# Performance work log

Measured on AMD Instinct MI355X. Metric: run time of the kernel, lower is better.

Reference implementation:

```python
import jax, jax.numpy as jnp
import numpy as np

EMBED_DIM = 1024
NUM_HEADS = 16
HEAD_DIM = EMBED_DIM // NUM_HEADS  # 64
SCALING = 0.125
T, B = 2048, 2


def setup_inputs() -> dict:
    key = jax.random.key(0)
    k_q, k_len, k_w1, k_b1, k_w2, k_b2 = jax.random.split(key, 6)
    query = jax.random.normal(k_q, (T, B, EMBED_DIM), dtype=jnp.float32)
    # realistic padding: each sequence has a valid length in [T//2, T)
    lengths = jax.random.randint(k_len, (B,), T // 2, T)
    key_padding_mask = jnp.arange(T)[None, :] >= lengths[:, None]  # [B, T] bool, True = pad
    s1 = 1.0 / np.sqrt(EMBED_DIM)
    W_in = jax.random.uniform(k_w1, (3 * EMBED_DIM, EMBED_DIM), jnp.float32, -s1, s1)
    b_in = jax.random.uniform(k_b1, (3 * EMBED_DIM,), jnp.float32, -s1, s1)
    W_out = jax.random.uniform(k_w2, (EMBED_DIM, EMBED_DIM), jnp.float32, -s1, s1)
    b_out = jax.random.uniform(k_b2, (EMBED_DIM,), jnp.float32, -s1, s1)
    return {"query": query, "key_padding_mask": key_padding_mask,
            "W_in": W_in, "b_in": b_in, "W_out": W_out, "b_out": b_out}


def reference(query, key_padding_mask, W_in, b_in, W_out, b_out):
    # query: [T, B, E]; key_padding_mask: [B, S] bool (True = padded key)
    t, b, e = query.shape
    h, hd = NUM_HEADS, HEAD_DIM
    proj = query @ W_in.T + b_in                      # [T, B, 3E]
    q, k, v = jnp.split(proj, 3, axis=-1)             # each [T, B, E]
    q = q * SCALING

    def to_bh(x):  # [T, B, E] -> [B*H, T, hd], matching torch view+transpose
        return x.reshape(t, b * h, hd).transpose(1, 0, 2)

    q, k, v = to_bh(q), to_bh(k), to_bh(v)
    attn_weights = jnp.einsum('bth,bsh->bts', q, k)   # [B*H, T, S]
    attn_weights = attn_weights.reshape(b, h, t, t)
    attn_weights = jnp.where(key_padding_mask[:, None, None, :], -jnp.inf, attn_weights)
    # softmax computed in float32 then cast back, as in the original
    attn_weights = jax.nn.softmax(attn_weights.astype(jnp.float32), axis=-1).astype(query.dtype)
    # dropout p=0 (eval/inference) -> identity
    attn = jnp.einsum('bhts,bhsd->bhtd', attn_weights, v.reshape(b, h, t, hd))  # [B,H,T,hd]
    attn = attn.reshape(b * h, t, hd).transpose(1, 0, 2).reshape(t, b, e)       # [T,B,E]
    return attn @ W_out.T + b_out
```

## Files before the change

kernel.cpp:

```cpp
#include <hip/hip_runtime.h>
#include <hip/hip_bf16.h>
#include <stdint.h>
#include <stddef.h>

typedef __hip_bfloat16 bf16;
typedef __attribute__((ext_vector_type(4))) float f32x4;
typedef __attribute__((ext_vector_type(8))) short s16x8;
typedef __attribute__((ext_vector_type(4))) short s16x4;

#define AS1 __attribute__((address_space(1)))
#define AS3 __attribute__((address_space(3)))

__device__ __forceinline__ void async_ld16(const void* g, void* l) {
  __builtin_amdgcn_global_load_lds((AS1 void*)g, (AS3 void*)l, 16, 0, 0);
}

#if __has_builtin(__builtin_amdgcn_exp2f)
#define EXP2F(x) __builtin_amdgcn_exp2f(x)
#else
#define EXP2F(x) exp2f(x)
#endif

__device__ __forceinline__ unsigned pk_bf16(float a, float b) {
  unsigned ua = __builtin_bit_cast(unsigned, a);
  unsigned ub = __builtin_bit_cast(unsigned, b);
  ua += 0x7FFFu + ((ua >> 16) & 1u);
  ub += 0x7FFFu + ((ub >> 16) & 1u);
  return (ua >> 16) | (ub & 0xFFFF0000u);
}

__device__ __forceinline__ unsigned pk_trunc(float a, float b) {
  return __builtin_amdgcn_perm(__builtin_bit_cast(unsigned, b),
                               __builtin_bit_cast(unsigned, a), 0x07060302u);
}

__global__ __launch_bounds__(256) void convert_all_kernel(const float* __restrict__ q_src,
                                                          const float* __restrict__ wi_src,
                                                          const float* __restrict__ wo_src,
                                                          bf16* __restrict__ q_dst,
                                                          bf16* __restrict__ wi_dst,
                                                          bf16* __restrict__ wo_dst,
                                                          const void* __restrict__ mask,
                                                          int* __restrict__ lengths) {
  int blk = blockIdx.x;
  if (blk >= 4096) {
    __shared__ int s_any;
    __shared__ int s_cnt[256];
    const int tid = threadIdx.x;
    const int b = blk - 4096;
    const unsigned char* m8 = (const unsigned char*)mask;
    if (tid == 0) s_any = 0;
    __syncthreads();
    int local = 0;
    for (int i = tid; i < 4096; i += 256) local |= m8[i];
    if (local) atomicOr(&s_any, 1);
    __syncthreads();
    int cnt = 0;
    if (s_any) {
      for (int t = tid; t < 2048; t += 256) cnt += (m8[b * 2048 + t] == 0) ? 1 : 0;
    } else {
      const int* m32 = (const int*)mask;
      for (int t = tid; t < 2048; t += 256) cnt += (m32[b * 2048 + t] == 0) ? 1 : 0;
    }
    s_cnt[tid] = cnt;
    __syncthreads();
    for (int s = 128; s > 0; s >>= 1) {
      if (tid < s) s_cnt[tid] += s_cnt[tid + s];
      __syncthreads();
    }
    if (tid == 0) lengths[b] = s_cnt[0];
    return;
  }
  const float* src;
  bf16* dst;
  int base;
  if (blk < 2048)      { src = q_src;  dst = q_dst;  base = blk * 2048; }
  else if (blk < 3584) { src = wi_src; dst = wi_dst; base = (blk - 2048) * 2048; }
  else                 { src = wo_src; dst = wo_dst; base = (blk - 3584) * 2048; }
  int i = base + threadIdx.x * 8;
  float4 a = *(const float4*)(src + i);
  float4 b = *(const float4*)(src + i + 4);
  unsigned u[4];
  u[0] = pk_bf16(a.x, a.y); u[1] = pk_bf16(a.z, a.w);
  u[2] = pk_bf16(b.x, b.y); u[3] = pk_bf16(b.z, b.w);
  *(uint4*)(dst + i) = *(const uint4*)u;
}

__global__ __launch_bounds__(256, 5) void gemm_qkv(const bf16* __restrict__ X,
                                                   const bf16* __restrict__ W,
                                                   const float* __restrict__ bias,
                                                   bf16* __restrict__ Qd,
                                                   bf16* __restrict__ Kd,
                                                   bf16* __restrict__ Vt) {
  __shared__ bf16 smem[(64 + 128) * 64];
  bf16* As = smem;
  bf16* Bs = smem + 4096;
  const int K = 1024;
  const int id = blockIdx.x;
  const int mt = id & 63, nt = id >> 6;
  const int m0 = mt * 64, n0 = nt * 128;
  const int tid = threadIdx.x;
  const int wave = tid >> 6, lane = tid & 63;
  const int col = lane & 15, quad = lane >> 4;
  const int wm = wave & 1, wn = wave >> 1;

  f32x4 acc[2][4];
#pragma unroll
  for (int mi = 0; mi < 2; mi++)
#pragma unroll
    for (int ni = 0; ni < 4; ni++) acc[mi][ni] = (f32x4){0.f, 0.f, 0.f, 0.f};

  const bf16* gA[2];
  char* ldA[2];
#pragma unroll
  for (int i = 0; i < 2; i++) {
    const int c = tid + 256 * i;
    const int row = c >> 3;
    const int j = (c & 7) ^ (row & 7);
    gA[i] = X + (size_t)(m0 + row) * K + j * 8;
    ldA[i] = (char*)As + (size_t)(wave * 64 + 256 * i) * 16;
  }
  const bf16* gB[4];
  char* ldB[4];
#pragma unroll
  for (int i = 0; i < 4; i++) {
    const int c = tid + 256 * i;
    const int row = c >> 3;
    const int j = (c & 7) ^ (row & 7);
    gB[i] = W + (size_t)(n0 + row) * K + j * 8;
    ldB[i] = (char*)Bs + (size_t)(wave * 64 + 256 * i) * 16;
  }

  for (int k0 = 0; k0 < K; k0 += 64) {
#pragma unroll
    for (int i = 0; i < 2; i++) async_ld16(gA[i] + k0, ldA[i]);
#pragma unroll
    for (int i = 0; i < 4; i++) async_ld16(gB[i] + k0, ldB[i]);
    __syncthreads();
#pragma unroll
    for (int kh = 0; kh < 2; kh++) {
      s16x8 af[2], bfr[4];
#pragma unroll
      for (int mi = 0; mi < 2; mi++) {
        const int arow = wm * 32 + mi * 16 + col;
        af[mi] = *(const s16x8*)((char*)As + arow * 128 + ((((kh << 2) | quad) ^ (arow & 7)) << 4));
      }
#pragma unroll
      for (int ni = 0; ni < 4; ni++) {
        const int brow = wn * 64 + ni * 16 + col;
        bfr[ni] = *(const s16x8*)((char*)Bs + brow * 128 + ((((kh << 2) | quad) ^ (brow & 7)) << 4));
      }
#pragma unroll
      for (int mi = 0; mi < 2; mi++)
#pragma unroll
        for (int ni = 0; ni < 4; ni++)
          acc[mi][ni] = __builtin_amdgcn_mfma_f32_16x16x32_bf16(af[mi], bfr[ni], acc[mi][ni], 0, 0, 0);
    }
    __syncthreads();
  }

  const float QSCALE = 0.125f * 1.4426950408889634f;
  if (nt < 16) {
    bf16* dstb = (nt < 8) ? Qd : Kd;
    const float sc = (nt < 8) ? QSCALE : 1.0f;
#pragma unroll
    for (int mi = 0; mi < 2; mi++)
#pragma unroll
      for (int ni = 0; ni < 4; ni++)
#pragma unroll
        for (int r = 0; r < 4; r++) {
          int m = m0 + wm * 32 + mi * 16 + quad * 4 + r;
          int n = n0 + wn * 64 + ni * 16 + col;
          float v = (acc[mi][ni][r] + bias[n]) * sc;
          int e = n & 1023, hh = e >> 6, d = e & 63;
          int t = m >> 1, b = m & 1;
          int bh = b * 16 + hh;
          dstb[((size_t)bh * 2048 + t) * 64 + d] = __float2bfloat16(v);
        }
  } else {
    const int hh0 = (nt - 16) * 2;
#pragma unroll
    for (int mi = 0; mi < 2; mi++) {
      const int s0 = wm * 16 + mi * 8 + quad * 2;
      const int off0 = ((s0 >> 2) & 3) * 8 + (s0 >> 4) * 4 + (s0 & 3);
#pragma unroll
      for (int ni = 0; ni < 4; ni++) {
        const int n = n0 + wn * 64 + ni * 16 + col;
        const float bv = bias[n];
        const int dfull = wn * 64 + ni * 16 + col;
        const int hh_rel = dfull >> 6, dd = dfull & 63;
#pragma unroll
        for (int b = 0; b < 2; b++) {
          float v0 = acc[mi][ni][b] + bv;
          float v1 = acc[mi][ni][b + 2] + bv;
          const int p = b * 2 + hh_rel;
          *(unsigned*)((char*)smem + ((p * 2048) + dd * 32 + off0) * 2) = pk_bf16(v0, v1);
        }
      }
    }
    __syncthreads();
    const int bh = (wave >> 1) * 16 + hh0 + (wave & 1);
    bf16* dstp = Vt + (size_t)bh * 131072 + mt * 2048;
    const char* srcp = (const char*)smem + wave * 4096;
#pragma unroll
    for (int jj = 0; jj < 4; jj++) {
      s16x8 v = *(const s16x8*)(srcp + jj * 1024 + lane * 16);
      *(s16x8*)(dstp + jj * 512 + lane * 8) = v;
    }
  }
}

__global__ __launch_bounds__(512, 4) void attn_kernel(const bf16* __restrict__ Qd,
                                                      const bf16* __restrict__ Kd,
                                                      const bf16* __restrict__ Vt,
                                                      const int* __restrict__ lengths,
                                                      bf16* __restrict__ attn_out) {
  __shared__ bf16 Ks[2][2][64 * 64];
  __shared__ bf16 Vs[2][2][64 * 64];

  const int id = blockIdx.x;
  const int slot = id >> 3;
  const int bh = (id & 7) * 4 + (slot & 3);
  const int qt0 = (slot >> 2) * 128;
  const int b = bh >> 4, h = bh & 15;

  const int tid = threadIdx.x;
  const int wave = tid >> 6, lane = tid & 63;
  const int half = wave >> 2, hw = wave & 3;
  const int col = lane & 15, quad = lane >> 4;
  const int len = lengths[b];
  const int nfull = len >> 6;
  const int rem = len & 63;
  const int nkt = nfull + (rem ? 1 : 0);
  const int nh0 = (nkt + 1) >> 1;
  const int first = half ? nh0 : 0;
  const int cnt = half ? (nkt - nh0) : nh0;

  s16x8 bq[2][2];
#pragma unroll
  for (int g = 0; g < 2; g++) {
    const bf16* qptr =
        Qd + ((size_t)bh * 2048 + qt0 + hw * 32 + g * 16 + col) * 64 + quad * 8;
    bq[g][0] = *(const s16x8*)(qptr);
    bq[g][1] = *(const s16x8*)(qptr + 32);
  }

  const int kbase0 = col * 128 + ((quad ^ (col & 7)) << 4);
  const int kbase1 = kbase0 ^ 64;
  const int HBUF = half * 16384;

  const bf16* Kg = Kd + (size_t)bh * 2048 * 64;
  const bf16* Vg = Vt + (size_t)bh * 131072;
  const int c0 = hw * 128 + lane, c1 = c0 + 64;
  const int r0 = c0 >> 3, j0 = (c0 & 7) ^ (r0 & 7);
  const int r1 = c1 >> 3, j1 = (c1 & 7) ^ (r1 & 7);
  const bf16* gK0 = Kg + r0 * 64 + j0 * 8;
  const bf16* gK1 = Kg + r1 * 64 + j1 * 8;
  const bf16* gV0 = Vg + (j0 >> 2) * 2048 + r0 * 32 + (j0 & 3) * 8;
  const bf16* gV1 = Vg + (j1 >> 2) * 2048 + r1 * 32 + (j1 & 3) * 8;
  const int dst0 = (hw * 128) * 16, dst1 = (hw * 128 + 64) * 16;

  auto stage = [&](int kt, int BUF) {
    const int off = kt * 4096;
    async_ld16(gK0 + off, (char*)Ks + BUF + dst0);
    async_ld16(gK1 + off, (char*)Ks + BUF + dst1);
    async_ld16(gV0 + off, (char*)Vs + BUF + dst0);
    async_ld16(gV1 + off, (char*)Vs + BUF + dst1);
  };

  const s16x4 aOnes = {0x3F80, 0x3F80, 0x3F80, 0x3F80};
  const f32x4 Zf = (f32x4){0.f, 0.f, 0.f, 0.f};
  f32x4 lacc[2] = {Zf, Zf};
  f32x4 oaccT[2][4];
#pragma unroll
  for (int g = 0; g < 2; g++)
#pragma unroll
    for (int dt = 0; dt < 4; dt++) oaccT[g][dt] = Zf;

  auto score = [&](int BUF, f32x4 (&s0)[4], f32x4 (&s1)[4]) {
#pragma unroll
    for (int ti = 0; ti < 4; ti++) {
      const s16x8 ak0 = *(const s16x8*)((char*)Ks + BUF + ti * 2048 + kbase0);
      s0[ti] = __builtin_amdgcn_mfma_f32_16x16x32_bf16(ak0, bq[0][0], Zf, 0, 0, 0);
      s1[ti] = __builtin_amdgcn_mfma_f32_16x16x32_bf16(ak0, bq[1][0], Zf, 0, 0, 0);
      const s16x8 ak1 = *(const s16x8*)((char*)Ks + BUF + ti * 2048 + kbase1);
      s0[ti] = __builtin_amdgcn_mfma_f32_16x16x32_bf16(ak1, bq[0][1], s0[ti], 0, 0, 0);
      s1[ti] = __builtin_amdgcn_mfma_f32_16x16x32_bf16(ak1, bq[1][1], s1[ti], 0, 0, 0);
    }
  };
  auto accum = [&](int BUF, s16x4 (&bP0)[4], s16x4 (&bP1)[4]) {
#pragma unroll
    for (int ti = 0; ti < 4; ti++) {
      lacc[0] = __builtin_amdgcn_mfma_f32_16x16x16bf16_1k(aOnes, bP0[ti], lacc[0], 0, 0, 0);
      lacc[1] = __builtin_amdgcn_mfma_f32_16x16x16bf16_1k(aOnes, bP1[ti], lacc[1], 0, 0, 0);
    }
#pragma unroll
    for (int dt = 0; dt < 4; dt++) {
#pragma unroll
      for (int sh = 0; sh < 2; sh++) {
        const s16x8 av = *(const s16x8*)((char*)Vs + BUF + dt * 2048 + (sh ? kbase1 : kbase0));
        const s16x4 alo = __builtin_shufflevector(av, av, 0, 1, 2, 3);
        const s16x4 ahi = __builtin_shufflevector(av, av, 4, 5, 6, 7);
        oaccT[0][dt] = __builtin_amdgcn_mfma_f32_16x16x16bf16_1k(alo, bP0[sh * 2], oaccT[0][dt], 0, 0, 0);
        oaccT[0][dt] = __builtin_amdgcn_mfma_f32_16x16x16bf16_1k(ahi, bP0[sh * 2 + 1], oaccT[0][dt], 0, 0, 0);
        oaccT[1][dt] = __builtin_amdgcn_mfma_f32_16x16x16bf16_1k(alo, bP1[sh * 2], oaccT[1][dt], 0, 0, 0);
        oaccT[1][dt] = __builtin_amdgcn_mfma_f32_16x16x16bf16_1k(ahi, bP1[sh * 2 + 1], oaccT[1][dt], 0, 0, 0);
      }
    }
  };

  auto tile_full = [&](int BUF) {
    f32x4 s0[4], s1[4];
    score(BUF, s0, s1);
    s16x4 bP0[4], bP1[4];
#pragma unroll
    for (int ti = 0; ti < 4; ti++) {
      uint2 u0 = {pk_trunc(EXP2F(s0[ti][0]), EXP2F(s0[ti][1])),
                  pk_trunc(EXP2F(s0[ti][2]), EXP2F(s0[ti][3]))};
      bP0[ti] = __builtin_bit_cast(s16x4, u0);
      uint2 u1 = {pk_trunc(EXP2F(s1[ti][0]), EXP2F(s1[ti][1])),
                  pk_trunc(EXP2F(s1[ti][2]), EXP2F(s1[ti][3]))};
      bP1[ti] = __builtin_bit_cast(s16x4, u1);
    }
    accum(BUF, bP0, bP1);
  };

  auto tile_mask = [&](int BUF) {
    f32x4 s0[4], s1[4];
    score(BUF, s0, s1);
    s16x4 bP0[4], bP1[4];
#pragma unroll
    for (int ti = 0; ti < 4; ti++) {
      const int sb = ti * 16 + quad * 4;
      float a0 = (sb + 0 < rem) ? EXP2F(s0[ti][0]) : 0.f;
      float a1 = (sb + 1 < rem) ? EXP2F(s0[ti][1]) : 0.f;
      float a2 = (sb + 2 < rem) ? EXP2F(s0[ti][2]) : 0.f;
      float a3 = (sb + 3 < rem) ? EXP2F(s0[ti][3]) : 0.f;
      uint2 u0 = {pk_trunc(a0, a1), pk_trunc(a2, a3)};
      bP0[ti] = __builtin_bit_cast(s16x4, u0);
      float c0m = (sb + 0 < rem) ? EXP2F(s1[ti][0]) : 0.f;
      float c1m = (sb + 1 < rem) ? EXP2F(s1[ti][1]) : 0.f;
      float c2m = (sb + 2 < rem) ? EXP2F(s1[ti][2]) : 0.f;
      float c3m = (sb + 3 < rem) ? EXP2F(s1[ti][3]) : 0.f;
      uint2 u1 = {pk_trunc(c0m, c1m), pk_trunc(c2m, c3m)};
      bP1[ti] = __builtin_bit_cast(s16x4, u1);
    }
    accum(BUF, bP0, bP1);
  };

  stage(first, HBUF);
  __syncthreads();
  for (int i = 0; i < nh0; i++) {
    if (i + 1 < cnt) stage(first + i + 1, HBUF + ((i + 1) & 1) * 8192);
    if (i < cnt) {
      const int kt = first + i;
      const int BUF = HBUF + (i & 1) * 8192;
      if (kt < nfull) tile_full(BUF); else tile_mask(BUF);
    }
    __syncthreads();
  }

  float* OF = (float*)Ks;
  float* LF = (float*)Vs;
  const int me = hw * 64 + lane;
  if (half == 1) {
#pragma unroll
    for (int g = 0; g < 2; g++) {
      LF[g * 256 + me] = lacc[g][0];
#pragma unroll
      for (int dt = 0; dt < 4; dt++)
#pragma unroll
        for (int r = 0; r < 4; r++)
          OF[(g * 16 + dt * 4 + r) * 256 + me] = oaccT[g][dt][r];
    }
  }
  __syncthreads();
  if (half == 0) {
#pragma unroll
    for (int g = 0; g < 2; g++) {
      const float linv = 1.0f / (lacc[g][0] + LF[g * 256 + me]);
      const int t = qt0 + hw * 32 + g * 16 + col;
      bf16* outp = attn_out + ((size_t)t * 2 + b) * 1024 + h * 64 + quad * 4;
#pragma unroll
      for (int dt = 0; dt < 4; dt++) {
        float o0 = (oaccT[g][dt][0] + OF[(g * 16 + dt * 4 + 0) * 256 + me]) * linv;
        float o1 = (oaccT[g][dt][1] + OF[(g * 16 + dt * 4 + 1) * 256 + me]) * linv;
        float o2 = (oaccT[g][dt][2] + OF[(g * 16 + dt * 4 + 2) * 256 + me]) * linv;
        float o3 = (oaccT[g][dt][3] + OF[(g * 16 + dt * 4 + 3) * 256 + me]) * linv;
        uint2 u = {pk_bf16(o0, o1), pk_bf16(o2, o3)};
        *(uint2*)(outp + dt * 16) = u;
      }
    }
  }
}

__global__ __launch_bounds__(256) void gemm_out(const bf16* __restrict__ Aa,
                                                const bf16* __restrict__ W,
                                                const float* __restrict__ bias,
                                                float* __restrict__ out) {
  __shared__ bf16 Bs[128 * 64];
  __shared__ bf16 As[64 * 64];
  const int K = 1024;
  const int m0 = blockIdx.y * 64, n0 = blockIdx.x * 128;
  const int tid = threadIdx.x;
  const int wave = tid >> 6, lane = tid & 63;
  const int col = lane & 15, quad = lane >> 4;

  f32x4 acc[8];
#pragma unroll
  for (int ni = 0; ni < 8; ni++) acc[ni] = (f32x4){0.f, 0.f, 0.f, 0.f};

  const bf16* gB[4];
  char* ldsB[4];
#pragma unroll
  for (int i = 0; i < 4; i++) {
    const int c = tid + 256 * i;
    const int row = c >> 3;
    const int j = (c & 7) ^ (row & 7);
    gB[i] = W + (size_t)(n0 + row) * K + j * 8;
    ldsB[i] = (char*)Bs + (size_t)(wave * 64 + 256 * i) * 16;
  }
  const bf16* gA[2];
  char* ldsA[2];
#pragma unroll
  for (int i = 0; i < 2; i++) {
    const int c = tid + 256 * i;
    const int row = c >> 3;
    const int j = (c & 7) ^ (row & 7);
    gA[i] = Aa + (size_t)(m0 + row) * K + j * 8;
    ldsA[i] = (char*)As + (size_t)(wave * 64 + 256 * i) * 16;
  }

  for (int k0 = 0; k0 < K; k0 += 64) {
#pragma unroll
    for (int i = 0; i < 4; i++) async_ld16(gB[i] + k0, ldsB[i]);
#pragma unroll
    for (int i = 0; i < 2; i++) async_ld16(gA[i] + k0, ldsA[i]);
    __syncthreads();
    const int arow = wave * 16 + col;
    const int abase = arow * 128 + ((quad ^ (arow & 7)) << 4);
    const s16x8 af0 = *(const s16x8*)((char*)As + abase);
    const s16x8 af1 = *(const s16x8*)((char*)As + (abase ^ 64));
#pragma unroll
    for (int ni = 0; ni < 8; ni++) {
      const int brow = ni * 16 + col;
      const int bbase = brow * 128 + ((quad ^ (brow & 7)) << 4);
      const s16x8 b0 = *(const s16x8*)((char*)Bs + bbase);
      acc[ni] = __builtin_amdgcn_mfma_f32_16x16x32_bf16(af0, b0, acc[ni], 0, 0, 0);
      const s16x8 b1 = *(const s16x8*)((char*)Bs + (bbase ^ 64));
      acc[ni] = __builtin_amdgcn_mfma_f32_16x16x32_bf16(af1, b1, acc[ni], 0, 0, 0);
    }
    __syncthreads();
  }

#pragma unroll
  for (int ni = 0; ni < 8; ni++)
#pragma unroll
    for (int r = 0; r < 4; r++) {
      int m = m0 + wave * 16 + quad * 4 + r;
      int n = n0 + ni * 16 + col;
      out[(size_t)m * 1024 + n] = acc[ni][r] + bias[n];
    }
}

extern "C" void kernel_launch(void* const* d_in, const int* in_sizes, int n_in,
                              void* d_out, int out_size, void* d_ws, size_t ws_size,
                              hipStream_t stream) {
  (void)in_sizes; (void)n_in; (void)out_size; (void)ws_size;
  const float* query = (const float*)d_in[0];
  const void*  mask  = d_in[1];
  const float* W_in  = (const float*)d_in[2];
  const float* b_in  = (const float*)d_in[3];
  const float* W_out = (const float*)d_in[4];
  const float* b_out = (const float*)d_in[5];
  float* out = (float*)d_out;

  char* ws = (char*)d_ws;
  bf16* Xbf    = (bf16*)(ws);
  bf16* attnb  = (bf16*)(ws);
  bf16* Winbf  = (bf16*)(ws + 8388608);
  bf16* Woutbf = (bf16*)(ws + 8388608 + 6291456);
  bf16* Qd     = (bf16*)(ws + 16777216);
  bf16* Kd     = (bf16*)(ws + 25165824);
  bf16* Vt     = (bf16*)(ws + 33554432);
  int*  lens   = (int*)(ws + 41943040);

  convert_all_kernel<<<4098, 256, 0, stream>>>(query, W_in, W_out, Xbf, Winbf, Woutbf,
                                               mask, lens);
  gemm_qkv<<<1536, 256, 0, stream>>>(Xbf, Winbf, b_in, Qd, Kd, Vt);
  attn_kernel<<<512, 512, 0, stream>>>(Qd, Kd, Vt, lens, attnb);
  gemm_out<<<dim3(8, 64), 256, 0, stream>>>(attnb, Woutbf, b_out, out);
}
```

Before: 183.5 us.

## Shrink output GEMM tile to 64x64 with 2x2 wave layout

Reworks the output-projection GEMM from 64x128 tiles, where each wave owned a 16x128 strip, to 64x64 tiles where each wave owns a 32x32 sub-tile as a 2x2 grid of MFMA blocks. The grid doubles to 1024 blocks to fill more CUs on a 4096x1024 output. LDS per block is halved and launch bounds request 4 blocks per CU for occupancy. The trade-off is more total global/LDS traffic per output element and lower arithmetic intensity per block.

```diff
diff --git a/kernel.cpp b/kernel.cpp
--- a/kernel.cpp
+++ b/kernel.cpp
@@ -394,73 +394,78 @@
   }
 }
 
-__global__ __launch_bounds__(256) void gemm_out(const bf16* __restrict__ Aa,
-                                                const bf16* __restrict__ W,
-                                                const float* __restrict__ bias,
-                                                float* __restrict__ out) {
-  __shared__ bf16 Bs[128 * 64];
+__global__ __launch_bounds__(256, 4) void gemm_out(const bf16* __restrict__ Aa,
+                                                   const bf16* __restrict__ W,
+                                                   const float* __restrict__ bias,
+                                                   float* __restrict__ out) {
+  __shared__ bf16 Bs[64 * 64];
   __shared__ bf16 As[64 * 64];
   const int K = 1024;
-  const int m0 = blockIdx.y * 64, n0 = blockIdx.x * 128;
+  const int m0 = blockIdx.y * 64, n0 = blockIdx.x * 64;
   const int tid = threadIdx.x;
   const int wave = tid >> 6, lane = tid & 63;
   const int col = lane & 15, quad = lane >> 4;
-
-  f32x4 acc[8];
-#pragma unroll
-  for (int ni = 0; ni < 8; ni++) acc[ni] = (f32x4){0.f, 0.f, 0.f, 0.f};
-
-  const bf16* gB[4];
-  char* ldsB[4];
-#pragma unroll
-  for (int i = 0; i < 4; i++) {
-    const int c = tid + 256 * i;
-    const int row = c >> 3;
-    const int j = (c & 7) ^ (row & 7);
-    gB[i] = W + (size_t)(n0 + row) * K + j * 8;
-    ldsB[i] = (char*)Bs + (size_t)(wave * 64 + 256 * i) * 16;
-  }
+  const int wm = wave & 1, wn = wave >> 1;
+
+  f32x4 acc[2][2];
+#pragma unroll
+  for (int mi = 0; mi < 2; mi++)
+#pragma unroll
+    for (int ni = 0; ni < 2; ni++) acc[mi][ni] = (f32x4){0.f, 0.f, 0.f, 0.f};
+
   const bf16* gA[2];
-  char* ldsA[2];
+  const bf16* gB[2];
+  char* ldA[2];
+  char* ldB[2];
 #pragma unroll
   for (int i = 0; i < 2; i++) {
     const int c = tid + 256 * i;
     const int row = c >> 3;
     const int j = (c & 7) ^ (row & 7);
     gA[i] = Aa + (size_t)(m0 + row) * K + j * 8;
-    ldsA[i] = (char*)As + (size_t)(wave * 64 + 256 * i) * 16;
+    gB[i] = W + (size_t)(n0 + row) * K + j * 8;
+    ldA[i] = (char*)As + (size_t)(wave * 64 + 256 * i) * 16;
+    ldB[i] = (char*)Bs + (size_t)(wave * 64 + 256 * i) * 16;
   }
 
   for (int k0 = 0; k0 < K; k0 += 64) {
 #pragma unroll
-    for (int i = 0; i < 4; i++) async_ld16(gB[i] + k0, ldsB[i]);
-#pragma unroll
-    for (int i = 0; i < 2; i++) async_ld16(gA[i] + k0, ldsA[i]);
-    __syncthreads();
-    const int arow = wave * 16 + col;
-    const int abase = arow * 128 + ((quad ^ (arow & 7)) << 4);
-    const s16x8 af0 = *(const s16x8*)((char*)As + abase);
-    const s16x8 af1 = *(const s16x8*)((char*)As + (abase ^ 64));
-#pragma unroll
-    for (int ni = 0; ni < 8; ni++) {
-      const int brow = ni * 16 + col;
-      const int bbase = brow * 128 + ((quad ^ (brow & 7)) << 4);
-      const s16x8 b0 = *(const s16x8*)((char*)Bs + bbase);
-      acc[ni] = __builtin_amdgcn_mfma_f32_16x16x32_bf16(af0, b0, acc[ni], 0, 0, 0);
-      const s16x8 b1 = *(const s16x8*)((char*)Bs + (bbase ^ 64));
-      acc[ni] = __builtin_amdgcn_mfma_f32_16x16x32_bf16(af1, b1, acc[ni], 0, 0, 0);
-    }
-    __syncthreads();
-  }
-
-#pragma unroll
-  for (int ni = 0; ni < 8; ni++)
-#pragma unroll
-    for (int r = 0; r < 4; r++) {
-      int m = m0 + wave * 16 + quad * 4 + r;
-      int n = n0 + ni * 16 + col;
-      out[(size_t)m * 1024 + n] = acc[ni][r] + bias[n];
-    }
+    for (int i = 0; i < 2; i++) async_ld16(gA[i] + k0, ldA[i]);
+#pragma unroll
+    for (int i = 0; i < 2; i++) async_ld16(gB[i] + k0, ldB[i]);
+    __syncthreads();
+#pragma unroll
+    for (int kh = 0; kh < 2; kh++) {
+      s16x8 af[2], bfr[2];
+#pragma unroll
+      for (int mi = 0; mi < 2; mi++) {
+        const int arow = wm * 32 + mi * 16 + col;
+        af[mi] = *(const s16x8*)((char*)As + arow * 128 + ((((kh << 2) | quad) ^ (arow & 7)) << 4));
+      }
+#pragma unroll
+      for (int ni = 0; ni < 2; ni++) {
+        const int brow = wn * 32 + ni * 16 + col;
+        bfr[ni] = *(const s16x8*)((char*)Bs + brow * 128 + ((((kh << 2) | quad) ^ (brow & 7)) << 4));
+      }
+#pragma unroll
+      for (int mi = 0; mi < 2; mi++)
+#pragma unroll
+        for (int ni = 0; ni < 2; ni++)
+          acc[mi][ni] = __builtin_amdgcn_mfma_f32_16x16x32_bf16(af[mi], bfr[ni], acc[mi][ni], 0, 0, 0);
+    }
+    __syncthreads();
+  }
+
+#pragma unroll
+  for (int mi = 0; mi < 2; mi++)
+#pragma unroll
+    for (int ni = 0; ni < 2; ni++)
+#pragma unroll
+      for (int r = 0; r < 4; r++) {
+        int m = m0 + wm * 32 + mi * 16 + quad * 4 + r;
+        int n = n0 + wn * 32 + ni * 16 + col;
+        out[(size_t)m * 1024 + n] = acc[mi][ni][r] + bias[n];
+      }
 }
 
 extern "C" void kernel_launch(void* const* d_in, const int* in_sizes, int n_in,
@@ -489,5 +494,5 @@
                                                mask, lens);
   gemm_qkv<<<1536, 256, 0, stream>>>(Xbf, Winbf, b_in, Qd, Kd, Vt);
   attn_kernel<<<512, 512, 0, stream>>>(Qd, Kd, Vt, lens, attnb);
-  gemm_out<<<dim3(8, 64), 256, 0, stream>>>(attnb, Woutbf, b_out, out);
-}
+  gemm_out<<<dim3(16, 64), 256, 0, stream>>>(attnb, Woutbf, b_out, out);
+}
```

New measurement: 182.7 us. About the same (-0.4%).
